# Optimization experiments

Hardware: AMD Instinct MI355X
Metric: run time of the kernel (lower is better)

Reference implementation:

```python
import jax, jax.numpy as jnp
import numpy as np

T, D, FF, E, K = 512, 2048, 768, 128, 8


def setup_inputs() -> dict:
    key = jax.random.key(0)
    k0, k1, k2, k3, k4 = jax.random.split(key, 5)
    scale = 0.02
    return {
        "hidden_states": jax.random.normal(k0, (T, D), dtype=jnp.float32),
        "w_gate": jax.random.normal(k1, (D, E), dtype=jnp.float32) * scale,  # router
        "w_gate_proj": jax.random.normal(k2, (E, D, FF), dtype=jnp.float32) * scale,
        "w_up_proj": jax.random.normal(k3, (E, D, FF), dtype=jnp.float32) * scale,
        "w_down_proj": jax.random.normal(k4, (E, FF, D), dtype=jnp.float32) * scale,
    }


def reference(hidden_states, w_gate, w_gate_proj, w_up_proj, w_down_proj):
    x = hidden_states  # [T, D]
    # Router: linear -> softmax (fp32) -> top-k -> renormalize (norm_topk_prob=True)
    router_logits = jnp.dot(x, w_gate)  # [T, E]
    probs = jax.nn.softmax(router_logits.astype(jnp.float32), axis=-1)
    topk_w, topk_idx = jax.lax.top_k(probs, K)  # [T, K]
    topk_w = topk_w / jnp.sum(topk_w, axis=-1, keepdims=True)
    topk_w = topk_w.astype(x.dtype)
    # Scatter per-(token,expert) combine weights: [T, E]
    rows = jnp.arange(T)[:, None]
    combine = jnp.zeros((T, E), dtype=x.dtype).at[rows, topk_idx].add(topk_w)
    # Grouped SwiGLU experts: scan over experts, weighted accumulation.
    def body(acc, per_expert):
        wg, wu, wd, s = per_expert  # [D,FF], [D,FF], [FF,D], [T]
        h = jax.nn.silu(jnp.dot(x, wg)) * jnp.dot(x, wu)  # [T, FF]
        return acc + s[:, None] * jnp.dot(h, wd), None

    init = jnp.zeros_like(x)
    out, _ = jax.lax.scan(
        body, init, (w_gate_proj, w_up_proj, w_down_proj, combine.T)
    )
    return out  # [T, D]
```

## Files before the change

kernel.cpp:

```cpp
#include <hip/hip_runtime.h>
#include <hip/hip_bf16.h>

#define TT 512
#define DH 2048
#define FFD 768
#define NE 128
#define TOPK 8
#define CAP 512
#define SMAX 64

typedef __attribute__((ext_vector_type(4))) float f32x4;
typedef __attribute__((ext_vector_type(8))) short short8;

typedef __attribute__((address_space(3))) unsigned int lds_u32_t;
typedef __attribute__((address_space(1))) unsigned int glob_u32_t;

__device__ __forceinline__ short f2bf(float f) {
    __hip_bfloat16 h = __float2bfloat16(f);
    return *reinterpret_cast<short*>(&h);
}

__device__ __forceinline__ void glds16(const float* g, float* l) {
    __builtin_amdgcn_global_load_lds((glob_u32_t*)g, (lds_u32_t*)l, 16, 0, 0);
}
__device__ __forceinline__ void glds16nt(const float* g, float* l) {
    __builtin_amdgcn_global_load_lds((glob_u32_t*)g, (lds_u32_t*)l, 16, 0, 2 );
}

template<int N>
__device__ __forceinline__ void vmwait() {
    asm volatile("s_waitcnt vmcnt(%0)" :: "i"(N) : "memory");
}

__global__ __launch_bounds__(128) void moe_init(int* __restrict__ cnt)
{
    cnt[threadIdx.x] = 0;
}

__global__ __launch_bounds__(128) void moe_router(
    const float* __restrict__ x, const float* __restrict__ wg,
    int* __restrict__ cnt, int* __restrict__ tok_list, float* __restrict__ w_list,
    float* __restrict__ out)
{
    const int t = blockIdx.x;
    const int e = threadIdx.x;
    __shared__ float xs[DH];
    __shared__ float red[NE];
    __shared__ int   redi[NE];
    __shared__ float selw[TOPK];
    __shared__ int   seli[TOPK];

    float4* outrow = (float4*)(out + (size_t)t * DH);
    const float4 z4 = make_float4(0.f, 0.f, 0.f, 0.f);
    #pragma unroll
    for (int i = 0; i < 4; ++i) outrow[e + i * 128] = z4;

    for (int i = e; i < DH; i += 128) xs[i] = x[(size_t)t * DH + i];
    __syncthreads();

    float acc = 0.f;
    #pragma unroll 4
    for (int d = 0; d < DH; ++d)
        acc = fmaf(xs[d], wg[(size_t)d * NE + e], acc);

    red[e] = acc; __syncthreads();
    for (int s = 64; s > 0; s >>= 1) {
        if (e < s) red[e] = fmaxf(red[e], red[e + s]);
        __syncthreads();
    }
    const float mx = red[0];
    __syncthreads();

    float myp = __expf(acc - mx);

    for (int k = 0; k < TOPK; ++k) {
        red[e] = myp; redi[e] = e;
        __syncthreads();
        for (int s = 64; s > 0; s >>= 1) {
            if (e < s) {
                const float v2 = red[e + s]; const int i2 = redi[e + s];
                if (v2 > red[e] || (v2 == red[e] && i2 < redi[e])) { red[e] = v2; redi[e] = i2; }
            }
            __syncthreads();
        }
        if (e == 0) { selw[k] = red[0]; seli[k] = redi[0]; }
        __syncthreads();
        if (e == seli[k]) myp = -1.f;
        __syncthreads();
    }

    if (e == 0) {
        float s8 = 0.f;
        #pragma unroll
        for (int k = 0; k < TOPK; ++k) s8 += selw[k];
        const float inv = 1.f / s8;
        #pragma unroll
        for (int k = 0; k < TOPK; ++k) {
            const int ex = seli[k];
            const float wv = selw[k] * inv;
            const int pos = atomicAdd(&cnt[ex], 1);
            if (pos < CAP) {
                tok_list[ex * CAP + pos] = t * TOPK + k;
                w_list[ex * CAP + pos] = wv;
            }
        }
    }
}

__global__ __launch_bounds__(256) void moe_gather(
    const float* __restrict__ x, const int* __restrict__ cnt,
    const int* __restrict__ tok_list, short* __restrict__ xgb)
{
    const int e = blockIdx.x;
    int n = cnt[e]; if (n > SMAX) n = SMAX;
    const int s0 = blockIdx.y * 8;
    const int k = threadIdx.x * 8;
    short* dste = xgb + (size_t)e * SMAX * DH;
    #pragma unroll
    for (int i = 0; i < 8; ++i) {
        const int s = s0 + i;
        short8 o = {0, 0, 0, 0, 0, 0, 0, 0};
        if (s < n) {
            const float* xr = x + (size_t)(tok_list[e * CAP + s] >> 3) * DH + k;
            const float4 v0 = *(const float4*)(xr);
            const float4 v1 = *(const float4*)(xr + 4);
            o[0] = f2bf(v0.x); o[1] = f2bf(v0.y); o[2] = f2bf(v0.z); o[3] = f2bf(v0.w);
            o[4] = f2bf(v1.x); o[5] = f2bf(v1.y); o[6] = f2bf(v1.z); o[7] = f2bf(v1.w);
        }
        *(short8*)(dste + (size_t)s * DH + k) = o;
    }
}

__global__ __launch_bounds__(64) void moe_gateup(
    const short* __restrict__ xgb,
    const float* __restrict__ wgp, const float* __restrict__ wup,
    short* __restrict__ hc)
{
    __shared__ __align__(16) float Bsh[6 * 2048];

    const int e = blockIdx.y;
    const int lane = threadIdx.x;
    const int fl = lane & 15;
    const int g16 = lane >> 4;
    const int koff = g16 * 8;
    const int f0 = blockIdx.x * 64;
    const int lrow = lane >> 4;
    const int lcol = (lane & 15) * 4;

    const short* xge = xgb + (size_t)e * SMAX * DH;
    const float* wgs = wgp + (size_t)e * DH * FFD + f0;
    const float* wus = wup + (size_t)e * DH * FFD + f0;

    f32x4 accg[4][4] = {};
    f32x4 accu[4][4] = {};
    short8 A0[4], A1[4], A2[4];

    auto ISSUE = [&](int t, int buf) {
        const int kk = t * 32;
        float* bg = &Bsh[buf * 2048];
        float* bu = &Bsh[6144 + buf * 2048];
        #pragma unroll
        for (int g = 0; g < 8; ++g) {
            const size_t ro = (size_t)(kk + g * 4 + lrow) * FFD + lcol;
            glds16nt(wgs + ro, bg + g * 256);
            glds16nt(wus + ro, bu + g * 256);
        }
    };
    auto LOADA = [&](int t, short8 (&a)[4]) {
        const int kk = t * 32 + koff;
        #pragma unroll
        for (int fm = 0; fm < 4; ++fm)
            a[fm] = *(const short8*)(xge + (size_t)(fm * 16 + fl) * DH + kk);
    };
    auto COMP = [&](int buf, const short8 (&a)[4]) {
        const float* bg = &Bsh[buf * 2048 + koff * 64 + fl];
        const float* bu = &Bsh[6144 + buf * 2048 + koff * 64 + fl];
        #pragma unroll
        for (int nf = 0; nf < 4; ++nf) {
            short8 bfg, bfu;
            #pragma unroll
            for (int j = 0; j < 8; ++j) {
                bfg[j] = f2bf(bg[nf * 16 + j * 64]);
                bfu[j] = f2bf(bu[nf * 16 + j * 64]);
            }
            #pragma unroll
            for (int fm = 0; fm < 4; ++fm) {
                accg[nf][fm] = __builtin_amdgcn_mfma_f32_16x16x32_bf16(a[fm], bfg, accg[nf][fm], 0, 0, 0);
                accu[nf][fm] = __builtin_amdgcn_mfma_f32_16x16x32_bf16(a[fm], bfu, accu[nf][fm], 0, 0, 0);
            }
        }
    };

    LOADA(0, A0); ISSUE(0, 0);
    LOADA(1, A1); ISSUE(1, 1);
    for (int i = 0; i < 20; ++i) {
        const int t = 3 * i;
        LOADA(t + 2, A2); ISSUE(t + 2, 2); vmwait<40>(); COMP(0, A0);
        LOADA(t + 3, A0); ISSUE(t + 3, 0); vmwait<40>(); COMP(1, A1);
        LOADA(t + 4, A1); ISSUE(t + 4, 1); vmwait<40>(); COMP(2, A2);
    }
    LOADA(62, A2); ISSUE(62, 2); vmwait<40>(); COMP(0, A0);
    LOADA(63, A0); ISSUE(63, 0); vmwait<40>(); COMP(1, A1);
    vmwait<20>(); COMP(2, A2);
    vmwait<0>();  COMP(0, A0);

    short* hce = hc + (size_t)e * SMAX * FFD + f0;
    #pragma unroll
    for (int nf = 0; nf < 4; ++nf) {
        #pragma unroll
        for (int fm = 0; fm < 4; ++fm) {
            #pragma unroll
            for (int r = 0; r < 4; ++r) {
                const int s = fm * 16 + g16 * 4 + r;
                const float g = accg[nf][fm][r];
                const float u = accu[nf][fm][r];
                const float hv = (g / (1.f + __expf(-g))) * u;
                hce[(size_t)s * FFD + nf * 16 + fl] = f2bf(hv);
            }
        }
    }
}

__global__ __launch_bounds__(64) void moe_down(
    const short* __restrict__ hc, const float* __restrict__ wdp,
    const int* __restrict__ cnt, const int* __restrict__ tok_list,
    const float* __restrict__ w_list, float* __restrict__ out)
{
    __shared__ __align__(16) float Bsh[3 * 2048];

    const int e = blockIdx.y;
    int n = cnt[e]; if (n > SMAX) n = SMAX;
    if (n == 0) return;

    const int lane = threadIdx.x;
    const int fl = lane & 15;
    const int g16 = lane >> 4;
    const int koff = g16 * 8;
    const int d0 = blockIdx.x * 64;
    const int lrow = lane >> 4;
    const int lcol = (lane & 15) * 4;

    const short* hce = hc + (size_t)e * SMAX * FFD;
    const float* wds = wdp + (size_t)e * FFD * DH + d0;

    f32x4 acc[4][4] = {};
    short8 A0[4], A1[4], A2[4];

    auto ISSUE = [&](int t, int buf) {
        const int kk = t * 32;
        float* bd = &Bsh[buf * 2048];
        #pragma unroll
        for (int g = 0; g < 8; ++g) {
            const size_t ro = (size_t)(kk + g * 4 + lrow) * DH + lcol;
            glds16nt(wds + ro, bd + g * 256);
        }
    };
    auto LOADA = [&](int t, short8 (&a)[4]) {
        const int kk = t * 32 + koff;
        #pragma unroll
        for (int fm = 0; fm < 4; ++fm)
            a[fm] = *(const short8*)(hce + (size_t)(fm * 16 + fl) * FFD + kk);
    };
    auto COMP = [&](int buf, const short8 (&a)[4]) {
        const float* bp = &Bsh[buf * 2048 + koff * 64 + fl];
        #pragma unroll
        for (int nf = 0; nf < 4; ++nf) {
            short8 bf;
            #pragma unroll
            for (int j = 0; j < 8; ++j) bf[j] = f2bf(bp[nf * 16 + j * 64]);
            #pragma unroll
            for (int fm = 0; fm < 4; ++fm)
                acc[nf][fm] = __builtin_amdgcn_mfma_f32_16x16x32_bf16(a[fm], bf, acc[nf][fm], 0, 0, 0);
        }
    };

    LOADA(0, A0); ISSUE(0, 0);
    LOADA(1, A1); ISSUE(1, 1);
    for (int i = 0; i < 6; ++i) {
        const int t = 3 * i;
        LOADA(t + 2, A2); ISSUE(t + 2, 2); vmwait<24>(); COMP(0, A0);
        LOADA(t + 3, A0); ISSUE(t + 3, 0); vmwait<24>(); COMP(1, A1);
        LOADA(t + 4, A1); ISSUE(t + 4, 1); vmwait<24>(); COMP(2, A2);
    }
    LOADA(20, A2); ISSUE(20, 2); vmwait<24>(); COMP(0, A0);
    LOADA(21, A0); ISSUE(21, 0); vmwait<24>(); COMP(1, A1);
    LOADA(22, A1); ISSUE(22, 1); vmwait<24>(); COMP(2, A2);
    LOADA(23, A2); ISSUE(23, 2); vmwait<24>(); COMP(0, A0);
    vmwait<12>(); COMP(1, A1);
    vmwait<0>();  COMP(2, A2);

    #pragma unroll
    for (int nf = 0; nf < 4; ++nf) {
        #pragma unroll
        for (int fm = 0; fm < 4; ++fm) {
            #pragma unroll
            for (int r = 0; r < 4; ++r) {
                const int s = fm * 16 + g16 * 4 + r;
                if (s < n) {
                    const int t = tok_list[e * CAP + s] >> 3;
                    const float wt = w_list[e * CAP + s];
                    atomicAdd(out + (size_t)t * DH + d0 + nf * 16 + fl, acc[nf][fm][r] * wt);
                }
            }
        }
    }
}

extern "C" void kernel_launch(void* const* d_in, const int* in_sizes, int n_in,
                              void* d_out, int out_size, void* d_ws, size_t ws_size,
                              hipStream_t stream) {
    const float* x   = (const float*)d_in[0];
    const float* wg  = (const float*)d_in[1];
    const float* wgp = (const float*)d_in[2];
    const float* wup = (const float*)d_in[3];
    const float* wdp = (const float*)d_in[4];
    float* out = (float*)d_out;

    char* ws = (char*)d_ws;
    int*   cnt      = (int*)ws;
    int*   tok_list = (int*)(ws + 1024);
    float* w_list   = (float*)(ws + 1024 + NE * CAP * 4);
    short* xgb      = (short*)(ws + (1 << 20));
    short* hc       = (short*)(ws + (1 << 20) + (size_t)NE * SMAX * DH * 2);

    moe_init<<<1, 128, 0, stream>>>(cnt);
    moe_router<<<TT, 128, 0, stream>>>(x, wg, cnt, tok_list, w_list, out);
    moe_gather<<<dim3(NE, 8), 256, 0, stream>>>(x, cnt, tok_list, xgb);
    moe_gateup<<<dim3(FFD / 64, NE), 64, 0, stream>>>(xgb, wgp, wup, hc);
    moe_down<<<dim3(DH / 64, NE), 64, 0, stream>>>(hc, wdp, cnt, tok_list, w_list, out);
}
```

Measured before the change: 684.8 us.

## Replace down-proj atomics with per-slot partial buffer and reduction kernel

The down-projection kernel now writes each token-slot's weighted partial row into a dense partial buffer indexed by slot id (token*8+k), using vectorized float4 stores staged through LDS. A new reduce kernel sums the 8 partials per token into the output, which removes the scattered float atomicAdds and the output zeroing in the router. The gate/up kernel also stages its bf16 output through LDS so it can write coalesced 16-byte rows. This adds an extra kernel launch and a 16 MB partial buffer round trip. The partial buffer reuses the xgb region, which is safe only because gather's output is consumed before down runs.

Result: no change. 673.4 us (-1.7%).

```diff
diff --git a/kernel.cpp b/kernel.cpp
--- a/kernel.cpp
+++ b/kernel.cpp
@@ -31,6 +31,7 @@
 __device__ __forceinline__ void vmwait() {
     asm volatile("s_waitcnt vmcnt(%0)" :: "i"(N) : "memory");
 }
+#define LGKM0() do { asm volatile("s_waitcnt lgkmcnt(0)" ::: "memory"); __builtin_amdgcn_sched_barrier(0); } while (0)
 
 __global__ __launch_bounds__(128) void moe_init(int* __restrict__ cnt)
 {
@@ -39,8 +40,7 @@
 
 __global__ __launch_bounds__(128) void moe_router(
     const float* __restrict__ x, const float* __restrict__ wg,
-    int* __restrict__ cnt, int* __restrict__ tok_list, float* __restrict__ w_list,
-    float* __restrict__ out)
+    int* __restrict__ cnt, int* __restrict__ tok_list, float* __restrict__ w_list)
 {
     const int t = blockIdx.x;
     const int e = threadIdx.x;
@@ -49,11 +49,6 @@
     __shared__ int   redi[NE];
     __shared__ float selw[TOPK];
     __shared__ int   seli[TOPK];
-
-    float4* outrow = (float4*)(out + (size_t)t * DH);
-    const float4 z4 = make_float4(0.f, 0.f, 0.f, 0.f);
-    #pragma unroll
-    for (int i = 0; i < 4; ++i) outrow[e + i * 128] = z4;
 
     for (int i = e; i < DH; i += 128) xs[i] = x[(size_t)t * DH + i];
     __syncthreads();
@@ -204,27 +199,30 @@
     vmwait<20>(); COMP(2, A2);
     vmwait<0>();  COMP(0, A0);
 
-    short* hce = hc + (size_t)e * SMAX * FFD + f0;
-    #pragma unroll
-    for (int nf = 0; nf < 4; ++nf) {
-        #pragma unroll
-        for (int fm = 0; fm < 4; ++fm) {
+    short* S = (short*)Bsh;
+    #pragma unroll
+    for (int nf = 0; nf < 4; ++nf)
+        #pragma unroll
+        for (int fm = 0; fm < 4; ++fm)
             #pragma unroll
             for (int r = 0; r < 4; ++r) {
                 const int s = fm * 16 + g16 * 4 + r;
                 const float g = accg[nf][fm][r];
                 const float u = accu[nf][fm][r];
                 const float hv = (g / (1.f + __expf(-g))) * u;
-                hce[(size_t)s * FFD + nf * 16 + fl] = f2bf(hv);
-            }
-        }
-    }
+                S[s * 72 + nf * 16 + fl] = f2bf(hv);
+            }
+    LGKM0();
+    short* myrow = hc + (size_t)e * SMAX * FFD + (size_t)lane * FFD + f0;
+    #pragma unroll
+    for (int j = 0; j < 8; ++j)
+        *(short8*)(myrow + j * 8) = *(const short8*)(S + lane * 72 + j * 8);
 }
 
 __global__ __launch_bounds__(64) void moe_down(
     const short* __restrict__ hc, const float* __restrict__ wdp,
     const int* __restrict__ cnt, const int* __restrict__ tok_list,
-    const float* __restrict__ w_list, float* __restrict__ out)
+    const float* __restrict__ w_list, float* __restrict__ partial)
 {
     __shared__ __align__(16) float Bsh[3 * 2048];
 
@@ -289,21 +287,44 @@
     vmwait<12>(); COMP(1, A1);
     vmwait<0>();  COMP(2, A2);
 
-    #pragma unroll
-    for (int nf = 0; nf < 4; ++nf) {
-        #pragma unroll
-        for (int fm = 0; fm < 4; ++fm) {
+    float* P = (float*)Bsh;
+    #pragma unroll
+    for (int nf = 0; nf < 4; ++nf)
+        #pragma unroll
+        for (int fm = 0; fm < 4; ++fm)
             #pragma unroll
             for (int r = 0; r < 4; ++r) {
                 const int s = fm * 16 + g16 * 4 + r;
-                if (s < n) {
-                    const int t = tok_list[e * CAP + s] >> 3;
-                    const float wt = w_list[e * CAP + s];
-                    atomicAdd(out + (size_t)t * DH + d0 + nf * 16 + fl, acc[nf][fm][r] * wt);
-                }
-            }
-        }
-    }
+                P[s * 68 + nf * 16 + fl] = acc[nf][fm][r];
+            }
+    LGKM0();
+    if (lane < n) {
+        const int slotid = tok_list[e * CAP + lane];
+        const float wt = w_list[e * CAP + lane];
+        float* prow = partial + (size_t)slotid * DH + d0;
+        #pragma unroll
+        for (int j = 0; j < 16; ++j) {
+            float4 v = *(const float4*)(P + lane * 68 + j * 4);
+            v.x *= wt; v.y *= wt; v.z *= wt; v.w *= wt;
+            *(float4*)(prow + j * 4) = v;
+        }
+    }
+}
+
+__global__ __launch_bounds__(256) void moe_reduce(
+    const float4* __restrict__ partial, float4* __restrict__ out)
+{
+    const int i = blockIdx.x * 256 + threadIdx.x;
+    const int t = i >> 9;
+    const int d4 = i & 511;
+    const float4* p = partial + (size_t)t * 8 * 512 + d4;
+    float4 s = p[0];
+    #pragma unroll
+    for (int k = 1; k < 8; ++k) {
+        const float4 v = p[(size_t)k * 512];
+        s.x += v.x; s.y += v.y; s.z += v.z; s.w += v.w;
+    }
+    out[i] = s;
 }
 
 extern "C" void kernel_launch(void* const* d_in, const int* in_sizes, int n_in,
@@ -321,11 +342,13 @@
     int*   tok_list = (int*)(ws + 1024);
     float* w_list   = (float*)(ws + 1024 + NE * CAP * 4);
     short* xgb      = (short*)(ws + (1 << 20));
+    float* partial  = (float*)(ws + (1 << 20));
     short* hc       = (short*)(ws + (1 << 20) + (size_t)NE * SMAX * DH * 2);
 
     moe_init<<<1, 128, 0, stream>>>(cnt);
-    moe_router<<<TT, 128, 0, stream>>>(x, wg, cnt, tok_list, w_list, out);
+    moe_router<<<TT, 128, 0, stream>>>(x, wg, cnt, tok_list, w_list);
     moe_gather<<<dim3(NE, 8), 256, 0, stream>>>(x, cnt, tok_list, xgb);
     moe_gateup<<<dim3(FFD / 64, NE), 64, 0, stream>>>(xgb, wgp, wup, hc);
-    moe_down<<<dim3(DH / 64, NE), 64, 0, stream>>>(hc, wdp, cnt, tok_list, w_list, out);
-}
+    moe_down<<<dim3(DH / 64, NE), 64, 0, stream>>>(hc, wdp, cnt, tok_list, w_list, partial);
+    moe_reduce<<<1024, 256, 0, stream>>>((const float4*)partial, (float4*)out);
+}
```
